# Kernel optimization log

Hardware: AMD Instinct MI355X
Metric: run time of the kernel (lower is better)

The kernel has to match this reference:

```python
import jax, jax.numpy as jnp
import numpy as np

B, S, D, H, F = 8, 1024, 1024, 16, 4096
DH = D // H
EPS = 1e-8
NEG_INF = -1e30


def setup_inputs() -> dict:
    key = jax.random.key(0)
    ks = jax.random.split(key, 12)
    x = jax.random.normal(ks[0], (B, S, D), jnp.float32)
    # variable valid lengths in [S//2, S]; True = keep (valid token)
    lengths = jax.random.randint(ks[1], (B,), S // 2, S + 1)
    src_key_padding_mask = jnp.arange(S)[None, :] < lengths[:, None]
    rel_pos_bias = 0.02 * jax.random.normal(ks[2], (1, H, S, S), jnp.float32)
    w = lambda k, sh, std: std * jax.random.normal(k, sh, jnp.float32)
    std = D ** -0.5
    return {
        'x': x,
        'src_key_padding_mask': src_key_padding_mask,
        'rel_pos_bias': rel_pos_bias,
        'Wq': w(ks[3], (D, D), std),
        'Wk': w(ks[4], (D, D), std),
        'Wv': w(ks[5], (D, D), std),
        'Wo': w(ks[6], (D, D), std),
        'g1': jnp.ones((D,), jnp.float32),
        'g2': jnp.ones((D,), jnp.float32),
        'W1': w(ks[7], (D, F), std),
        'b1': jnp.zeros((F,), jnp.float32),
        'W2': w(ks[8], (F, F and D), F ** -0.5),
        'b2': jnp.zeros((D,), jnp.float32),
    }


def rmsnorm(x, g):
    # x / sqrt(mean(x^2) + eps) * g   (no mean subtraction)
    ms = jnp.mean(x * x, axis=-1, keepdims=True)
    return x * jax.lax.rsqrt(ms + EPS) * g


def attention(h, kpm, rel_pos_bias, Wq, Wk, Wv, Wo):
    b, s, d = h.shape
    q = (h @ Wq).reshape(b, s, H, DH)
    k = (h @ Wk).reshape(b, s, H, DH)
    v = (h @ Wv).reshape(b, s, H, DH)
    scores = jnp.einsum('bqhd,bkhd->bhqk', q, k) / np.sqrt(DH)
    scores = scores + rel_pos_bias
    scores = jnp.where(kpm[:, None, None, :], scores, NEG_INF)
    attn = jax.nn.softmax(scores, axis=-1)
    out = jnp.einsum('bhqk,bkhd->bqhd', attn, v).reshape(b, s, d)
    return out @ Wo


def reference(x, src_key_padding_mask, rel_pos_bias,
              Wq, Wk, Wv, Wo, g1, g2, W1, b1, W2, b2):
    h = rmsnorm(x, g1)
    x = x + attention(h, src_key_padding_mask, rel_pos_bias, Wq, Wk, Wv, Wo)
    h = rmsnorm(x, g2)
    ff = jax.nn.relu(h @ W1 + b1) @ W2 + b2
    return x + ff
```

## Files before the change

kernel.cpp:

```cpp
#include <hip/hip_runtime.h>
#include <stdint.h>

typedef __bf16 bf16;
typedef __bf16 bf16x4 __attribute__((ext_vector_type(4)));
typedef __bf16 bf16x8 __attribute__((ext_vector_type(8)));
typedef float f32x4 __attribute__((ext_vector_type(4)));

constexpr int Bz = 8, S = 1024, D = 1024, NH = 16, DH = 64, F = 4096;

__device__ __forceinline__ bool is_f32(const uint16_t* dt) { return dt[0] == 0; }

__device__ __forceinline__ void ld4(const void* p, size_t idx, bool f32, float o[4]) {
  if (f32) {
    float4 v = *(const float4*)((const float*)p + idx);
    o[0] = v.x; o[1] = v.y; o[2] = v.z; o[3] = v.w;
  } else {
    bf16x4 v = *(const bf16x4*)((const bf16*)p + idx);
    o[0] = v[0]; o[1] = v[1]; o[2] = v[2]; o[3] = v[3];
  }
}

__device__ __forceinline__ float ld1(const void* p, size_t idx, bool f32) {
  return f32 ? ((const float*)p)[idx] : (float)((const bf16*)p)[idx];
}

__device__ __forceinline__ void gload_lds16(const bf16* g, bf16* l) {
  __builtin_amdgcn_global_load_lds(
      (const __attribute__((address_space(1))) void*)g,
      (__attribute__((address_space(3))) void*)l, 16, 0, 0);
}

__global__ void prep_all(const void* __restrict__ sq, const void* __restrict__ sk,
                         const void* __restrict__ sv, const void* __restrict__ so,
                         const void* __restrict__ s1, const void* __restrict__ s2,
                         bf16* __restrict__ dq, bf16* __restrict__ dk,
                         bf16* __restrict__ dv, bf16* __restrict__ do_,
                         bf16* __restrict__ d1, bf16* __restrict__ d2,
                         const unsigned char* __restrict__ mask,
                         int* __restrict__ lengths,
                         const void* __restrict__ rpb, bf16* __restrict__ biasb,
                         const void* __restrict__ x, const void* __restrict__ g1,
                         bf16* __restrict__ hbuf,
                         const uint16_t* __restrict__ dt) {
  __shared__ bf16 tile[64][65];
  __shared__ int sred[4];
  __shared__ float sredf[4];
  bool f32 = is_f32(dt);
  int t = blockIdx.x;
  int tx = threadIdx.x, ty = threadIdx.y;
  int tid = ty * 16 + tx;
  if (t >= 19464) {
    int row = t - 19464;
    float xf[4];
    ld4(x, (size_t)row * D + tid * 4, f32, xf);
    float ss = xf[0] * xf[0] + xf[1] * xf[1] + xf[2] * xf[2] + xf[3] * xf[3];
#pragma unroll
    for (int m = 32; m >= 1; m >>= 1) ss += __shfl_xor(ss, m);
    if ((tid & 63) == 0) sredf[tid >> 6] = ss;
    __syncthreads();
    float tot = sredf[0] + sredf[1] + sredf[2] + sredf[3];
    float scale = rsqrtf(tot * (1.0f / D) + 1e-8f);
    float gf[4];
    ld4(g1, (size_t)tid * 4, f32, gf);
    bf16x4 ov;
#pragma unroll
    for (int j = 0; j < 4; j++) ov[j] = (bf16)(xf[j] * scale * gf[j]);
    *(bf16x4*)(hbuf + (size_t)row * D + tid * 4) = ov;
    return;
  }
  if (t >= 3080) {
    size_t i = ((size_t)(t - 3080) * 256 + tid) * 4;
    float v[4];
    ld4(rpb, i, f32, v);
    bf16x4 o;
#pragma unroll
    for (int j = 0; j < 4; j++) o[j] = (bf16)(v[j] * 1.4426950408889634f);
    *(bf16x4*)(biasb + i) = o;
    return;
  }
  if (t >= 3072) {
    int b = t - 3072;
    int esz = (mask[1] == 1) ? 1 : ((mask[1] != 0) ? 2 : 4);
    int cnt = 0;
    for (int s = tid; s < S; s += 256) {
      const unsigned char* p = mask + ((size_t)b * S + s) * esz;
      unsigned v = 0;
      for (int j = 0; j < esz; j++) v |= p[j];
      cnt += (v != 0) ? 1 : 0;
    }
#pragma unroll
    for (int m = 32; m >= 1; m >>= 1) cnt += __shfl_xor(cnt, m);
    if ((tid & 63) == 0) sred[tid >> 6] = cnt;
    __syncthreads();
    if (tid == 0) lengths[b] = sred[0] + sred[1] + sred[2] + sred[3];
    return;
  }
  const void* src;
  bf16* dst;
  int R, C, gx, base;
  if (t < 1024) {
    int wsel = t >> 8;
    base = wsel << 8;
    src = wsel == 0 ? sq : wsel == 1 ? sk : wsel == 2 ? sv : so;
    dst = wsel == 0 ? dq : wsel == 1 ? dk : wsel == 2 ? dv : do_;
    R = 1024; C = 1024; gx = 16;
  } else if (t < 2048) {
    base = 1024; src = s1; dst = d1; R = 1024; C = 4096; gx = 64;
  } else {
    base = 2048; src = s2; dst = d2; R = 4096; C = 1024; gx = 16;
  }
  int rel = t - base;
  int c0 = (rel % gx) * 64, r0 = (rel / gx) * 64;
#pragma unroll
  for (int i = 0; i < 4; i++) {
    int r = ty * 4 + i;
    float v[4];
    ld4(src, (size_t)(r0 + r) * C + c0 + tx * 4, f32, v);
#pragma unroll
    for (int j = 0; j < 4; j++) tile[r][tx * 4 + j] = (bf16)v[j];
  }
  __syncthreads();
#pragma unroll
  for (int i = 0; i < 4; i++) {
    int rr = ty * 4 + i;
    bf16x4 ov;
#pragma unroll
    for (int j = 0; j < 4; j++) ov[j] = tile[tx * 4 + j][rr];
    *(bf16x4*)(dst + (size_t)(c0 + rr) * R + r0 + tx * 4) = ov;
  }
}

template <bool ADD>
__global__ void rmsnorm_kernel(const void* __restrict__ xv, const bf16* __restrict__ add,
                               const void* __restrict__ gv, bf16* __restrict__ y,
                               const uint16_t* __restrict__ dt) {
  bool f32 = is_f32(dt);
  int row = blockIdx.x, t = threadIdx.x;
  float xf[4];
  ld4(xv, (size_t)row * D + t * 4, f32, xf);
  if (ADD) {
    bf16x4 a = *(const bf16x4*)(add + (size_t)row * D + t * 4);
#pragma unroll
    for (int j = 0; j < 4; j++) xf[j] += (float)a[j];
  }
  float ss = xf[0] * xf[0] + xf[1] * xf[1] + xf[2] * xf[2] + xf[3] * xf[3];
#pragma unroll
  for (int m = 32; m >= 1; m >>= 1) ss += __shfl_xor(ss, m);
  __shared__ float sred[4];
  if ((t & 63) == 0) sred[t >> 6] = ss;
  __syncthreads();
  float tot = sred[0] + sred[1] + sred[2] + sred[3];
  float scale = rsqrtf(tot * (1.0f / D) + 1e-8f);
  float gf[4];
  ld4(gv, (size_t)t * 4, f32, gf);
  bf16x4 ov;
#pragma unroll
  for (int j = 0; j < 4; j++) ov[j] = (bf16)(xf[j] * scale * gf[j]);
  *(bf16x4*)(y + (size_t)row * D + t * 4) = ov;
}

template <bool BIAS, bool RELU, bool RES1, bool RES2, bool OUTEXT, bool VT>
__global__ void gemm_nt(const bf16* __restrict__ A, const bf16* __restrict__ Bt,
                        void* __restrict__ Cv, const void* __restrict__ biasv,
                        const void* __restrict__ res1, const bf16* __restrict__ res2,
                        int M, int N, int K, const uint16_t* __restrict__ dt) {
  bool f32 = is_f32(dt);
  __shared__ bf16 As[4 * 4096];
  __shared__ bf16 Bs[4 * 4096];
  const int tid = threadIdx.x, lane = tid & 63, w = tid >> 6;
  const int wm = w >> 1, wn = w & 1;
  const int lid = blockIdx.x;
  const int bm = ((lid & 7) << 3) + ((lid >> 3) & 7);
  const int bn = lid >> 6;
  const int quad = lane >> 4, c = lane & 15;

  f32x4 acc[4][4];
#pragma unroll
  for (int i = 0; i < 4; i++)
#pragma unroll
    for (int j = 0; j < 4; j++)
#pragma unroll
      for (int r = 0; r < 4; r++) acc[i][j][r] = 0.f;

  const bf16* gA = A + (size_t)(bm * 128 + w * 16 + (lane >> 2)) * K + (lane & 3) * 8;
  const bf16* gB = Bt + (size_t)(bn * 128 + w * 16 + (lane >> 2)) * K + (lane & 3) * 8;
  bf16* lA = As + w * 512;
  bf16* lB = Bs + w * 512;
  const size_t rstep = (size_t)64 * K;

  int aoff[4], boff[4];
#pragma unroll
  for (int i = 0; i < 4; i++) {
    aoff[i] = (wm * 64 + i * 16 + c) * 32 + quad * 8;
    boff[i] = (wn * 64 + i * 16 + c) * 32 + quad * 8;
  }

  for (int k0 = 0; k0 < K; k0 += 128) {
    __syncthreads();
#pragma unroll
    for (int p = 0; p < 4; p++) {
      gload_lds16(gA + p * 32, lA + p * 4096);
      gload_lds16(gA + p * 32 + rstep, lA + p * 4096 + 2048);
      gload_lds16(gB + p * 32, lB + p * 4096);
      gload_lds16(gB + p * 32 + rstep, lB + p * 4096 + 2048);
    }
    gA += 128;
    gB += 128;
    __syncthreads();
#pragma unroll
    for (int p = 0; p < 4; p++) {
      bf16x8 af[4], bfr[4];
#pragma unroll
      for (int i = 0; i < 4; i++) af[i] = *(const bf16x8*)(As + p * 4096 + aoff[i]);
#pragma unroll
      for (int i = 0; i < 4; i++) bfr[i] = *(const bf16x8*)(Bs + p * 4096 + boff[i]);
#pragma unroll
      for (int i = 0; i < 4; i++)
#pragma unroll
        for (int j = 0; j < 4; j++)
          acc[i][j] = __builtin_amdgcn_mfma_f32_16x16x32_bf16(af[i], bfr[j], acc[i][j], 0, 0, 0);
    }
  }

  const int m0 = bm * 128 + wm * 64, n0 = bn * 128 + wn * 64;
#pragma unroll
  for (int i = 0; i < 4; i++) {
#pragma unroll
    for (int j = 0; j < 4; j++) {
      int col = n0 + j * 16 + c;
      if (VT) {
        int row0 = m0 + i * 16 + quad * 4;
        int bb = row0 >> 10, s0 = row0 & 1023;
        int hh = col >> 6, dd = col & 63;
        bf16x4 ov;
#pragma unroll
        for (int r = 0; r < 4; r++) ov[r] = (bf16)acc[i][j][r];
        *(bf16x4*)((bf16*)Cv + ((size_t)((bb << 4) + hh) * 64 + dd) * 1024 + s0) = ov;
      } else {
        float bv = BIAS ? ld1(biasv, col, f32) : 0.f;
#pragma unroll
        for (int r = 0; r < 4; r++) {
          int row = m0 + i * 16 + quad * 4 + r;
          size_t idx = (size_t)row * N + col;
          float vv = acc[i][j][r] + bv;
          if (RELU) vv = fmaxf(vv, 0.f);
          if (RES1) vv += ld1(res1, idx, f32);
          if (RES2) vv += (float)res2[idx];
          if (OUTEXT && f32) ((float*)Cv)[idx] = vv;
          else ((bf16*)Cv)[idx] = (bf16)vv;
        }
      }
    }
  }
}

#define SYNC()                            \
  do {                                    \
    __builtin_amdgcn_sched_barrier(0);    \
    __builtin_amdgcn_s_barrier();         \
    __builtin_amdgcn_sched_barrier(0);    \
  } while (0)
#define VMW(n)                                              \
  do {                                                      \
    asm volatile("s_waitcnt vmcnt(" #n ")" ::: "memory");   \
    __builtin_amdgcn_sched_barrier(0);                      \
  } while (0)

#define STA_(nb, rowbase, kb)                                                  \
  do {                                                                         \
    gload_lds16(Ag + (size_t)(rowbase) * K + (kb), &Abuf[nb][(rowbase) * 64]); \
    gload_lds16(Ag + (size_t)((rowbase) + 8) * K + (kb),                       \
                &Abuf[nb][((rowbase) + 8) * 64]);                              \
  } while (0)
#define STB_(nb, rowbase, kb)                                                  \
  do {                                                                         \
    gload_lds16(Bg + (size_t)(rowbase) * K + (kb), &Bbuf[nb][(rowbase) * 64]); \
    gload_lds16(Bg + (size_t)((rowbase) + 8) * K + (kb),                       \
                &Bbuf[nb][((rowbase) + 8) * 64]);                              \
  } while (0)
#define RDA_(MQ, fr, bufsel)                                                          \
  do {                                                                                \
    _Pragma("unroll") for (int ii = 0; ii < 4; ii++) {                                \
      int arow = wm * 128 + ((MQ)*4 + ii) * 16 + c;                                   \
      fr[ii][0] = *(const bf16x8*)&Abuf[bufsel][arow * 64 + ((quad ^ sx) * 8)];       \
      fr[ii][1] = *(const bf16x8*)&Abuf[bufsel][arow * 64 + (((4 + quad) ^ sx) * 8)]; \
    }                                                                                 \
  } while (0)
#define RDB_(NQ, fr, bufsel)                                                          \
  do {                                                                                \
    _Pragma("unroll") for (int jj = 0; jj < 2; jj++) {                                \
      int brow = wn * 64 + ((NQ)*2 + jj) * 16 + c;                                    \
      fr[jj][0] = *(const bf16x8*)&Bbuf[bufsel][brow * 64 + ((quad ^ sx) * 8)];       \
      fr[jj][1] = *(const bf16x8*)&Bbuf[bufsel][brow * 64 + (((4 + quad) ^ sx) * 8)]; \
    }                                                                                 \
  } while (0)

template <int MQ, int NQ>
__device__ __forceinline__ void mm_phase(f32x4 (&acc)[8][4], const bf16x8 (&afr)[4][2],
                                         const bf16x8 (&bfr)[2][2]) {
#pragma unroll
  for (int ii = 0; ii < 4; ii++)
#pragma unroll
    for (int jj = 0; jj < 2; jj++) {
      acc[MQ * 4 + ii][NQ * 2 + jj] = __builtin_amdgcn_mfma_f32_16x16x32_bf16(
          afr[ii][0], bfr[jj][0], acc[MQ * 4 + ii][NQ * 2 + jj], 0, 0, 0);
      acc[MQ * 4 + ii][NQ * 2 + jj] = __builtin_amdgcn_mfma_f32_16x16x32_bf16(
          afr[ii][1], bfr[jj][1], acc[MQ * 4 + ii][NQ * 2 + jj], 0, 0, 0);
    }
}

template <bool BIAS, bool RELU, bool QKV>
__global__ void __launch_bounds__(512, 2) gemm256(
    const bf16* __restrict__ A, const bf16* __restrict__ Bt, bf16* __restrict__ C,
    bf16* __restrict__ C2, const void* __restrict__ biasv, int N, int K,
    const uint16_t* __restrict__ dt) {
  bool f32 = is_f32(dt);
  __shared__ bf16 Abuf[2][256 * 64];
  __shared__ bf16 Bbuf[2][256 * 64];
  const int tid = threadIdx.x, lane = tid & 63, w = tid >> 6;
  const int wm = w >> 2, wn = w & 3;
  const int quad = lane >> 4, c = lane & 15;
  const int sx = c & 7;
  const int nbn = N >> 8;
  const int nwg = gridDim.x;
  const int sid = (blockIdx.x & 7) * (nwg >> 3) + (blockIdx.x >> 3);
  const int bm = sid / nbn, bn = sid % nbn;

  const int lrow = lane >> 3;
  const int lslot = ((lane & 7) ^ lrow) * 8;
  const bf16* Ag = A + (size_t)(bm * 256 + lrow) * K + lslot;
  const bf16* Bg = Bt + (size_t)(bn * 256 + lrow) * K + lslot;

  const int ra0 = wm * 128 + wn * 16;
  const int ra1 = ra0 + 64;
  const int rb0 = (wn >> 1) * 128 + (wn & 1) * 64 + wm * 16;
  const int rb1 = rb0 + 32;

  f32x4 acc[8][4];
#pragma unroll
  for (int i = 0; i < 8; i++)
#pragma unroll
    for (int j = 0; j < 4; j++)
#pragma unroll
      for (int r = 0; r < 4; r++) acc[i][j][r] = 0.f;

  const int nt = K >> 6;

  STA_(0, ra0, 0);
  STA_(0, ra1, 0);
  STB_(0, rb0, 0);
  STB_(0, rb1, 0);
  STA_(1, ra0, 64);
  VMW(2);
  SYNC();

  for (int t = 0; t < nt; ++t) {
    const int buf = t & 1, nb = buf ^ 1;
    const int kb1 = (t + 1) << 6, kb2 = (t + 2) << 6;
    const bool st1 = (t + 1 < nt), st2 = (t + 2 < nt);
    bf16x8 afr[4][2], bfr0[2][2], bfr1[2][2];
    RDA_(0, afr, buf);
    RDB_(0, bfr0, buf);
    if (st1) STA_(nb, ra1, kb1);
    SYNC();
    __builtin_amdgcn_s_setprio(1);
    mm_phase<0, 0>(acc, afr, bfr0);
    __builtin_amdgcn_s_setprio(0);
    VMW(2);
    SYNC();
    RDB_(1, bfr1, buf);
    if (st1) STB_(nb, rb0, kb1);
    SYNC();
    __builtin_amdgcn_s_setprio(1);
    mm_phase<0, 1>(acc, afr, bfr1);
    __builtin_amdgcn_s_setprio(0);
    SYNC();
    RDA_(1, afr, buf);
    if (st2) STA_(buf, ra0, kb2);
    SYNC();
    __builtin_amdgcn_s_setprio(1);
    mm_phase<1, 0>(acc, afr, bfr0);
    __builtin_amdgcn_s_setprio(0);
    SYNC();
    if (st1) STB_(nb, rb1, kb1);
    SYNC();
    __builtin_amdgcn_s_setprio(1);
    mm_phase<1, 1>(acc, afr, bfr1);
    __builtin_amdgcn_s_setprio(0);
    VMW(4);
    SYNC();
  }

  const int m0 = bm * 256 + wm * 128, n0 = bn * 256 + wn * 64;
  if (QKV && n0 >= 2048) {
#pragma unroll
    for (int fi = 0; fi < 8; fi++)
#pragma unroll
      for (int fj = 0; fj < 4; fj++) {
        int vcol = n0 + fj * 16 + c - 2048;
        int hh = vcol >> 6, dd = vcol & 63;
        int row0 = m0 + fi * 16 + quad * 4;
        int bb = row0 >> 10, s0 = row0 & 1023;
        bf16x4 ov;
#pragma unroll
        for (int r = 0; r < 4; r++) ov[r] = (bf16)acc[fi][fj][r];
        *(bf16x4*)(C2 + ((size_t)((bb << 4) + hh) * 64 + dd) * 1024 + s0) = ov;
      }
    return;
  }
  const int ldc = QKV ? 2048 : N;
#pragma unroll
  for (int fi = 0; fi < 8; fi++)
#pragma unroll
    for (int fj = 0; fj < 4; fj++) {
      int col = n0 + fj * 16 + c;
      float bv = BIAS ? ld1(biasv, col, f32) : 0.f;
#pragma unroll
      for (int r = 0; r < 4; r++) {
        int row = m0 + fi * 16 + quad * 4 + r;
        float vv = acc[fi][fj][r] + bv;
        if (RELU) vv = fmaxf(vv, 0.f);
        C[(size_t)row * ldc + col] = (bf16)vv;
      }
    }
}

__global__ void __launch_bounds__(256) attn_kernel(
    const bf16* __restrict__ qk, const bf16* __restrict__ vt,
    const bf16* __restrict__ bias, const int* __restrict__ lengths,
    bf16* __restrict__ out) {
  __shared__ bf16 QPs[64 * 72];
  __shared__ bf16 Ks[2][64][72];
  __shared__ bf16 Vs[2][64][72];
  const int tid = threadIdx.x, lane = tid & 63, w = tid >> 6;
  const int id = blockIdx.x;
  const int qt = id >> 7, b = (id >> 4) & 7, h = id & 15;
  const int len = lengths[b];
  const int quad = lane >> 4, c = lane & 15;
  const int r4 = tid >> 2, c4 = tid & 3;

  {
    size_t qrow = (size_t)(b * S + qt * 64 + r4) * 2048 + h * 64 + c4 * 8;
    *(bf16x8*)&QPs[r4 * 72 + c4 * 8] = *(const bf16x8*)&qk[qrow];
    *(bf16x8*)&QPs[r4 * 72 + 32 + c4 * 8] = *(const bf16x8*)&qk[qrow + 32];
  }
  __syncthreads();
  const bf16x8 a0 = *(const bf16x8*)&QPs[(w * 16 + c) * 72 + quad * 8];
  const bf16x8 a1 = *(const bf16x8*)&QPs[(w * 16 + c) * 72 + 32 + quad * 8];

  bf16* Pw = QPs + w * 16 * 72;
  const int xsw = (quad & 2) << 3;
  const int xsr = (c & 8) << 1;

  float l_[4] = {0.f, 0.f, 0.f, 0.f};
  f32x4 o[4];
#pragma unroll
  for (int ni = 0; ni < 4; ni++)
#pragma unroll
    for (int r = 0; r < 4; r++) o[ni][r] = 0.f;

  const bf16* bbp = bias + (size_t)h * S * S + (size_t)(qt * 64 + w * 16 + quad * 4) * S;
  const int nkt = (len + 63) >> 6;

  const size_t KSTEP = (size_t)64 * 2048;
  const bf16* gk = qk + (size_t)(b * S + r4) * 2048 + 1024 + h * 64 + c4 * 8;
  const bf16* gv = vt + ((size_t)((b * 16 + h) * 64 + r4)) * 1024 + c4 * 8;
  bf16x8 kr0 = *(const bf16x8*)gk;
  bf16x8 kr1 = *(const bf16x8*)(gk + 32);
  bf16x8 vr0 = *(const bf16x8*)gv;
  bf16x8 vr1 = *(const bf16x8*)(gv + 32);
  gk += KSTEP;
  gv += 64;
  *(bf16x8*)&Ks[0][r4][c4 * 8] = kr0;
  *(bf16x8*)&Ks[0][r4][32 + c4 * 8] = kr1;
  *(bf16x8*)&Vs[0][r4][c4 * 8] = vr0;
  *(bf16x8*)&Vs[0][r4][32 + c4 * 8] = vr1;
  if (nkt > 1) {
    kr0 = *(const bf16x8*)gk;
    kr1 = *(const bf16x8*)(gk + 32);
    vr0 = *(const bf16x8*)gv;
    vr1 = *(const bf16x8*)(gv + 32);
    gk += KSTEP;
    gv += 64;
  }
  __syncthreads();

  for (int kt = 0; kt < nkt; kt++) {
    const int buf = kt & 1, nb = buf ^ 1;
    if (kt + 1 < nkt) {
      *(bf16x8*)&Ks[nb][r4][c4 * 8] = kr0;
      *(bf16x8*)&Ks[nb][r4][32 + c4 * 8] = kr1;
      *(bf16x8*)&Vs[nb][r4][c4 * 8] = vr0;
      *(bf16x8*)&Vs[nb][r4][32 + c4 * 8] = vr1;
      if (kt + 2 < nkt) {
        kr0 = *(const bf16x8*)gk;
        kr1 = *(const bf16x8*)(gk + 32);
        vr0 = *(const bf16x8*)gv;
        vr1 = *(const bf16x8*)(gv + 32);
        gk += KSTEP;
        gv += 64;
      }
    }

    bf16 br[4][4];
#pragma unroll
    for (int ni = 0; ni < 4; ni++)
#pragma unroll
      for (int r = 0; r < 4; r++) br[ni][r] = bbp[(size_t)r * S + ni * 16 + c];

    f32x4 s[4];
#pragma unroll
    for (int ni = 0; ni < 4; ni++)
#pragma unroll
      for (int r = 0; r < 4; r++) s[ni][r] = 0.f;
    __builtin_amdgcn_s_setprio(1);
#pragma unroll
    for (int ni = 0; ni < 4; ni++) {
      bf16x8 b0 = *(const bf16x8*)&Ks[buf][ni * 16 + c][quad * 8];
      bf16x8 b1 = *(const bf16x8*)&Ks[buf][ni * 16 + c][32 + quad * 8];
      s[ni] = __builtin_amdgcn_mfma_f32_16x16x32_bf16(a0, b0, s[ni], 0, 0, 0);
      s[ni] = __builtin_amdgcn_mfma_f32_16x16x32_bf16(a1, b1, s[ni], 0, 0, 0);
    }
    __builtin_amdgcn_s_setprio(0);

    const bool full = (kt * 64 + 64 <= len);
#pragma unroll
    for (int ni = 0; ni < 4; ni++) {
      int col = kt * 64 + ni * 16 + c;
      bool valid = full || (col < len);
#pragma unroll
      for (int r = 0; r < 4; r++) {
        float p = valid ? exp2f(fmaf(s[ni][r], 0.18033688011112042f, (float)br[ni][r])) : 0.f;
        s[ni][r] = p;
        l_[r] += p;
      }
    }

#pragma unroll
    for (int ni = 0; ni < 4; ni++)
#pragma unroll
      for (int r = 0; r < 4; r++)
        Pw[(quad * 4 + r) * 72 + ((ni * 16 + c) ^ xsw)] = (bf16)s[ni][r];

    bf16x8 p0 = *(const bf16x8*)&Pw[c * 72 + ((quad * 8) ^ xsr)];
    bf16x8 p1 = *(const bf16x8*)&Pw[c * 72 + ((32 + quad * 8) ^ xsr)];
    __builtin_amdgcn_s_setprio(1);
#pragma unroll
    for (int ni = 0; ni < 4; ni++) {
      bf16x8 vb0 = *(const bf16x8*)&Vs[buf][ni * 16 + c][quad * 8];
      bf16x8 vb1 = *(const bf16x8*)&Vs[buf][ni * 16 + c][32 + quad * 8];
      o[ni] = __builtin_amdgcn_mfma_f32_16x16x32_bf16(p0, vb0, o[ni], 0, 0, 0);
      o[ni] = __builtin_amdgcn_mfma_f32_16x16x32_bf16(p1, vb1, o[ni], 0, 0, 0);
    }
    __builtin_amdgcn_s_setprio(0);
    bbp += 64;
    __syncthreads();
  }

  float inv[4];
#pragma unroll
  for (int r = 0; r < 4; r++) {
    float l = l_[r];
    l += __shfl_xor(l, 1);
    l += __shfl_xor(l, 2);
    l += __shfl_xor(l, 4);
    l += __shfl_xor(l, 8);
    inv[r] = 1.f / l;
  }
#pragma unroll
  for (int ni = 0; ni < 4; ni++)
#pragma unroll
    for (int r = 0; r < 4; r++) {
      size_t idx = ((size_t)(b * S + qt * 64 + w * 16 + quad * 4 + r)) * D + h * 64 + ni * 16 + c;
      out[idx] = (bf16)(o[ni][r] * inv[r]);
    }
}

extern "C" void kernel_launch(void* const* d_in, const int* in_sizes, int n_in,
                              void* d_out, int out_size, void* d_ws, size_t ws_size,
                              hipStream_t stream) {
  const void* x = d_in[0];
  const unsigned char* mask = (const unsigned char*)d_in[1];
  const void* rpb = d_in[2];
  const void* Wq = d_in[3];
  const void* Wk = d_in[4];
  const void* Wv = d_in[5];
  const void* Wo = d_in[6];
  const void* g1 = d_in[7];
  const void* g2 = d_in[8];
  const void* W1 = d_in[9];
  const void* b1 = d_in[10];
  const void* W2 = d_in[11];
  const void* b2 = d_in[12];
  const uint16_t* dt = (const uint16_t*)d_in[7];

  char* ws = (char*)d_ws;
  const size_t MB = 1024 * 1024;
  bf16* WqkT = (bf16*)(ws + 0 * MB);
  bf16* WkT = (bf16*)(ws + 2 * MB);
  bf16* WvT = (bf16*)(ws + 4 * MB);
  bf16* WoT = (bf16*)(ws + 6 * MB);
  bf16* W1T = (bf16*)(ws + 8 * MB);
  bf16* W2T = (bf16*)(ws + 16 * MB);
  bf16* hbuf = (bf16*)(ws + 24 * MB);
  bf16* qkbuf = (bf16*)(ws + 40 * MB);
  bf16* d1buf = (bf16*)(ws + 40 * MB);
  bf16* vtbuf = (bf16*)(ws + 72 * MB);
  bf16* biasb = (bf16*)(ws + 88 * MB);
  bf16* a1b = (bf16*)(ws + 56 * MB);
  int* lens = (int*)d_out;

  prep_all<<<dim3(3080 + 16384 + 8192), dim3(16, 16), 0, stream>>>(
      Wq, Wk, Wv, Wo, W1, W2, WqkT, WkT, WvT, WoT, W1T, W2T, mask, lens, rpb, biasb,
      x, g1, hbuf, dt);

  gemm256<false, false, true><<<dim3(384), dim3(512), 0, stream>>>(
      hbuf, WqkT, qkbuf, vtbuf, nullptr, 3072, 1024, dt);
  attn_kernel<<<dim3(2048), dim3(256), 0, stream>>>(qkbuf, vtbuf, biasb, lens, hbuf);
  gemm_nt<false, false, false, false, false, false><<<dim3(8 * 64), dim3(256), 0, stream>>>(
      hbuf, WoT, d1buf, nullptr, nullptr, nullptr, 8192, 1024, 1024, dt);
  rmsnorm_kernel<true><<<dim3(8192), dim3(256), 0, stream>>>(x, d1buf, g2, hbuf, dt);
  gemm256<true, true, false><<<dim3(512), dim3(512), 0, stream>>>(
      hbuf, W1T, a1b, nullptr, b1, 4096, 1024, dt);
  gemm_nt<true, false, true, true, true, false><<<dim3(8 * 64), dim3(256), 0, stream>>>(
      a1b, W2T, d_out, b2, x, d1buf, 8192, 1024, 4096, dt);

  (void)in_sizes; (void)n_in; (void)out_size; (void)ws_size;
}
```

Before: 524.7 us.

## Restructure GEMM LDS staging into half-tiles with two-iteration unrolled pipeline

Splits the A and B LDS buffers into per-half 128-row sub-tiles. Each wave now loads contiguous 8-row blocks with a per-row XOR swizzle instead of the earlier scattered row assignment. The main K loop is unrolled by two so the buffer indices are compile-time constants. Global-to-LDS issue is reordered so that B loads come before A loads, and vmcnt waits are adjusted per stage. The aim is to cut address arithmetic and improve load/compute overlap, at the cost of a more intricate schedule that assumes nt is even.

Result: slower. 537.0 us (+2.4%).

```diff
diff --git a/kernel.cpp b/kernel.cpp
--- a/kernel.cpp
+++ b/kernel.cpp
@@ -265,34 +265,36 @@
     asm volatile("s_waitcnt vmcnt(" #n ")" ::: "memory");   \
     __builtin_amdgcn_sched_barrier(0);                      \
   } while (0)
-
-#define STA_(nb, rowbase, kb)                                                  \
+#define PRIO1 __builtin_amdgcn_s_setprio(1)
+#define PRIO0 __builtin_amdgcn_s_setprio(0)
+
+#define STG_(G, Lb, half, kb)                                                  \
   do {                                                                         \
-    gload_lds16(Ag + (size_t)(rowbase) * K + (kb), &Abuf[nb][(rowbase) * 64]); \
-    gload_lds16(Ag + (size_t)((rowbase) + 8) * K + (kb),                       \
-                &Abuf[nb][((rowbase) + 8) * 64]);                              \
+    _Pragma("unroll") for (int j = 0; j < 2; j++) {                            \
+      int bi = j * 8 + w;                                                      \
+      int hr = bi * 8 + (lane >> 3);                                           \
+      gload_lds16(G + (size_t)((half)*128 + hr) * K + (kb) +                   \
+                      ((lane & 7) ^ (hr & 7)) * 8,                             \
+                  (Lb) + bi * 512);                                            \
+    }                                                                          \
   } while (0)
-#define STB_(nb, rowbase, kb)                                                  \
-  do {                                                                         \
-    gload_lds16(Bg + (size_t)(rowbase) * K + (kb), &Bbuf[nb][(rowbase) * 64]); \
-    gload_lds16(Bg + (size_t)((rowbase) + 8) * K + (kb),                       \
-                &Bbuf[nb][((rowbase) + 8) * 64]);                              \
-  } while (0)
-#define RDA_(MQ, fr, bufsel)                                                          \
+#define STGA(bufsel, half, kb) STG_(Ag, &Abuf[bufsel][half][0], half, kb)
+#define STGB(bufsel, half, kb) STG_(Bg, &Bbuf[bufsel][half][0], half, kb)
+#define RDA2(MQ, fr, bufsel)                                                          \
   do {                                                                                \
     _Pragma("unroll") for (int ii = 0; ii < 4; ii++) {                                \
-      int arow = wm * 128 + ((MQ)*4 + ii) * 16 + c;                                   \
-      fr[ii][0] = *(const bf16x8*)&Abuf[bufsel][arow * 64 + ((quad ^ sx) * 8)];       \
-      fr[ii][1] = *(const bf16x8*)&Abuf[bufsel][arow * 64 + (((4 + quad) ^ sx) * 8)]; \
+      int r = ((MQ)*4 + ii) * 16 + c;                                                 \
+      fr[ii][0] = *(const bf16x8*)&Abuf[bufsel][wm][r * 64 + ((quad ^ sx) * 8)];      \
+      fr[ii][1] = *(const bf16x8*)&Abuf[bufsel][wm][r * 64 + (((4 + quad) ^ sx) * 8)];\
     }                                                                                 \
   } while (0)
-#define RDB_(NQ, fr, bufsel)                                                          \
-  do {                                                                                \
-    _Pragma("unroll") for (int jj = 0; jj < 2; jj++) {                                \
-      int brow = wn * 64 + ((NQ)*2 + jj) * 16 + c;                                    \
-      fr[jj][0] = *(const bf16x8*)&Bbuf[bufsel][brow * 64 + ((quad ^ sx) * 8)];       \
-      fr[jj][1] = *(const bf16x8*)&Bbuf[bufsel][brow * 64 + (((4 + quad) ^ sx) * 8)]; \
-    }                                                                                 \
+#define RDB2(NQ, fr, bufsel)                                                           \
+  do {                                                                                 \
+    _Pragma("unroll") for (int jj = 0; jj < 2; jj++) {                                 \
+      int r = (wn & 1) * 64 + ((NQ)*2 + jj) * 16 + c;                                  \
+      fr[jj][0] = *(const bf16x8*)&Bbuf[bufsel][wn >> 1][r * 64 + ((quad ^ sx) * 8)];  \
+      fr[jj][1] = *(const bf16x8*)&Bbuf[bufsel][wn >> 1][r * 64 + (((4 + quad) ^ sx) * 8)]; \
+    }                                                                                  \
   } while (0)
 
 template <int MQ, int NQ>
@@ -315,8 +317,8 @@
     bf16* __restrict__ C2, const void* __restrict__ biasv, int N, int K,
     const uint16_t* __restrict__ dt) {
   bool f32 = is_f32(dt);
-  __shared__ bf16 Abuf[2][256 * 64];
-  __shared__ bf16 Bbuf[2][256 * 64];
+  __shared__ bf16 Abuf[2][2][128 * 64];
+  __shared__ bf16 Bbuf[2][2][128 * 64];
   const int tid = threadIdx.x, lane = tid & 63, w = tid >> 6;
   const int wm = w >> 2, wn = w & 3;
   const int quad = lane >> 4, c = lane & 15;
@@ -326,15 +328,8 @@
   const int sid = (blockIdx.x & 7) * (nwg >> 3) + (blockIdx.x >> 3);
   const int bm = sid / nbn, bn = sid % nbn;
 
-  const int lrow = lane >> 3;
-  const int lslot = ((lane & 7) ^ lrow) * 8;
-  const bf16* Ag = A + (size_t)(bm * 256 + lrow) * K + lslot;
-  const bf16* Bg = Bt + (size_t)(bn * 256 + lrow) * K + lslot;
-
-  const int ra0 = wm * 128 + wn * 16;
-  const int ra1 = ra0 + 64;
-  const int rb0 = (wn >> 1) * 128 + (wn & 1) * 64 + wm * 16;
-  const int rb1 = rb0 + 32;
+  const bf16* Ag = A + (size_t)(bm * 256) * K;
+  const bf16* Bg = Bt + (size_t)(bn * 256) * K;
 
   f32x4 acc[8][4];
 #pragma unroll
@@ -346,48 +341,85 @@
 
   const int nt = K >> 6;
 
-  STA_(0, ra0, 0);
-  STA_(0, ra1, 0);
-  STB_(0, rb0, 0);
-  STB_(0, rb1, 0);
-  STA_(1, ra0, 64);
-  VMW(2);
+  STGA(0, 0, 0);
+  STGA(0, 1, 0);
+  STGB(0, 0, 0);
+  STGB(0, 1, 0);
+  STGB(1, 0, 64);
+  STGA(1, 0, 64);
+  VMW(4);
   SYNC();
 
-  for (int t = 0; t < nt; ++t) {
-    const int buf = t & 1, nb = buf ^ 1;
-    const int kb1 = (t + 1) << 6, kb2 = (t + 2) << 6;
-    const bool st1 = (t + 1 < nt), st2 = (t + 2 < nt);
+  for (int i = 0; i < (nt >> 1); ++i) {
+    const int t1k = (i << 7) + 64;
+    const int k2 = (i << 7) + 128, k3 = (i << 7) + 192;
+    const bool s2 = (k2 < K), s3 = (k3 < K);
     bf16x8 afr[4][2], bfr0[2][2], bfr1[2][2];
-    RDA_(0, afr, buf);
-    RDB_(0, bfr0, buf);
-    if (st1) STA_(nb, ra1, kb1);
-    SYNC();
-    __builtin_amdgcn_s_setprio(1);
+    RDA2(0, afr, 0);
+    RDB2(0, bfr0, 0);
+    STGA(1, 1, t1k);
+    SYNC();
+    PRIO1;
     mm_phase<0, 0>(acc, afr, bfr0);
-    __builtin_amdgcn_s_setprio(0);
-    VMW(2);
-    SYNC();
-    RDB_(1, bfr1, buf);
-    if (st1) STB_(nb, rb0, kb1);
-    SYNC();
-    __builtin_amdgcn_s_setprio(1);
+    PRIO0;
+    SYNC();
+    RDB2(1, bfr1, 0);
+    STGB(1, 1, t1k);
+    SYNC();
+    PRIO1;
     mm_phase<0, 1>(acc, afr, bfr1);
-    __builtin_amdgcn_s_setprio(0);
-    SYNC();
-    RDA_(1, afr, buf);
-    if (st2) STA_(buf, ra0, kb2);
-    SYNC();
-    __builtin_amdgcn_s_setprio(1);
+    PRIO0;
+    SYNC();
+    RDA2(1, afr, 0);
+    if (s2) STGB(0, 0, k2);
+    SYNC();
+    PRIO1;
     mm_phase<1, 0>(acc, afr, bfr0);
-    __builtin_amdgcn_s_setprio(0);
-    SYNC();
-    if (st1) STB_(nb, rb1, kb1);
-    SYNC();
-    __builtin_amdgcn_s_setprio(1);
+    PRIO0;
+    SYNC();
+    if (s2) STGA(0, 0, k2);
+    SYNC();
+    PRIO1;
     mm_phase<1, 1>(acc, afr, bfr1);
-    __builtin_amdgcn_s_setprio(0);
-    VMW(4);
+    PRIO0;
+    if (s2) {
+      VMW(4);
+    } else {
+      VMW(0);
+    }
+    SYNC();
+    RDA2(0, afr, 1);
+    RDB2(0, bfr0, 1);
+    if (s2) STGA(0, 1, k2);
+    SYNC();
+    PRIO1;
+    mm_phase<0, 0>(acc, afr, bfr0);
+    PRIO0;
+    SYNC();
+    RDB2(1, bfr1, 1);
+    if (s2) STGB(0, 1, k2);
+    SYNC();
+    PRIO1;
+    mm_phase<0, 1>(acc, afr, bfr1);
+    PRIO0;
+    SYNC();
+    RDA2(1, afr, 1);
+    if (s3) STGB(1, 0, k3);
+    SYNC();
+    PRIO1;
+    mm_phase<1, 0>(acc, afr, bfr0);
+    PRIO0;
+    SYNC();
+    if (s3) STGA(1, 0, k3);
+    SYNC();
+    PRIO1;
+    mm_phase<1, 1>(acc, afr, bfr1);
+    PRIO0;
+    if (s3) {
+      VMW(4);
+    } else {
+      VMW(0);
+    }
     SYNC();
   }
 
```
